# Kernel tuning notes

Hardware: AMD Instinct MI355X
Metric: run time of the kernel (lower is better)

## Reference

```python
import jax, jax.numpy as jnp
import numpy as np

B, S = 2, 2048
HID, NH, NKV, HD = 4096, 32, 8, 128
THETA = 10000.0
WINDOW = 1024  # sliding window size


def setup_inputs() -> dict:
    key = jax.random.key(0)
    k1, k2, k3 = jax.random.split(key, 3)
    hidden_states = jax.random.normal(k1, (B, S, HID), jnp.float32)
    wqkv = jax.random.normal(k2, (HID, (NH + 2 * NKV) * HD), jnp.float32) * 0.02
    wo = jax.random.normal(k3, (NH * HD, HID), jnp.float32) * 0.02
    positions = jnp.arange(S, dtype=jnp.int32)
    return {"hidden_states": hidden_states, "wqkv": wqkv, "wo": wo, "positions": positions}


def _rope_neox(x, positions):
    # x: [B, S, h, HD]; GPT-NeoX style: rotate concatenated halves.
    half = HD // 2
    inv_freq = 1.0 / (THETA ** (jnp.arange(half, dtype=jnp.float32) / half))
    ang = positions.astype(jnp.float32)[:, None] * inv_freq  # [S, half]
    cos = jnp.cos(ang)[None, :, None, :]
    sin = jnp.sin(ang)[None, :, None, :]
    x1, x2 = jnp.split(x, 2, axis=-1)
    return jnp.concatenate([x1 * cos - x2 * sin, x2 * cos + x1 * sin], axis=-1)


def reference(hidden_states, wqkv, wo, positions):
    qkv = hidden_states @ wqkv  # [B, S, (NH+2*NKV)*HD]
    q, k, v = jnp.split(qkv, [NH * HD, NH * HD + NKV * HD], axis=-1)
    q = q.reshape(B, S, NH, HD)
    k = k.reshape(B, S, NKV, HD)
    v = v.reshape(B, S, NKV, HD)
    q = _rope_neox(q, positions)
    k = _rope_neox(k, positions)
    # GQA: each KV head serves NH // NKV query heads
    rep = NH // NKV
    k = jnp.repeat(k, rep, axis=2)  # [B, S, NH, HD]
    v = jnp.repeat(v, rep, axis=2)
    scale = HD ** -0.5
    scores = jnp.einsum('bqhd,bkhd->bhqk', q, k) * scale  # [B, NH, S, S]
    i = jnp.arange(S)[:, None]
    j = jnp.arange(S)[None, :]
    mask = (j <= i) & (i - j < WINDOW)  # causal + sliding window
    scores = jnp.where(mask[None, None], scores, jnp.float32(-1e30))
    probs = jax.nn.softmax(scores, axis=-1)
    attn = jnp.einsum('bhqk,bkhd->bqhd', probs, v).reshape(B, S, NH * HD)
    return attn @ wo  # [B, S, HID]
```

## Files before the change

kernel.cpp:

```cpp
#include <hip/hip_runtime.h>


typedef __attribute__((ext_vector_type(8))) short short8;
typedef __attribute__((ext_vector_type(4))) float f32x4;
typedef __attribute__((ext_vector_type(16))) float f32x16;
typedef __attribute__((ext_vector_type(4))) unsigned int u32x4;
typedef __attribute__((ext_vector_type(4))) unsigned short u16x4;

__device__ __forceinline__ unsigned short f2bf(float f) {
  unsigned int u = __builtin_bit_cast(unsigned int, f);
  u = u + 0x7fffu + ((u >> 16) & 1u);
  return (unsigned short)(u >> 16);
}
__device__ __forceinline__ float bf2f(unsigned short h) {
  unsigned int u = ((unsigned int)h) << 16;
  return __builtin_bit_cast(float, u);
}
__device__ __forceinline__ unsigned int cvtpk_bf16(float lo, float hi) {
  unsigned int r;
  asm("v_cvt_pk_bf16_f32 %0, %1, %2" : "=v"(r) : "v"(lo), "v"(hi));
  return r;
}

__device__ __forceinline__ void gload_lds16(const unsigned short* g, unsigned short* l) {
  __builtin_amdgcn_global_load_lds(
      (const __attribute__((address_space(1))) unsigned int*)g,
      (__attribute__((address_space(3))) unsigned int*)l, 16, 0, 0);
}

#define MFMA16(A, B, C) __builtin_amdgcn_mfma_f32_16x16x32_bf16((A), (B), (C), 0, 0, 0)
#define MFMA32(A, B, C) __builtin_amdgcn_mfma_f32_32x32x16_bf16((A), (B), (C), 0, 0, 0)
#define BC8(x) __builtin_bit_cast(short8, (x))

__global__ __launch_bounds__(256) void cvt_plain(const float* __restrict__ in,
                                                 unsigned short* __restrict__ out, int n) {
  const int i = (blockIdx.x * 256 + threadIdx.x) * 4;
  (void)n;
  f32x4 v = *(const f32x4*)(in + i);
  u16x4 o;
#pragma unroll
  for (int j = 0; j < 4; ++j) o[j] = f2bf(v[j]);
  *(u16x4*)(out + i) = o;
}

__global__ __launch_bounds__(256) void cvt_t(const float* __restrict__ in,
                                             unsigned short* __restrict__ out,
                                             int R, int C) {
  __shared__ float t[32][33];
  const int c0 = blockIdx.x * 32, r0 = blockIdx.y * 32;
  const int tx = threadIdx.x & 31, ty = threadIdx.x >> 5;
#pragma unroll
  for (int i = 0; i < 4; ++i)
    t[ty + i * 8][tx] = in[(size_t)(r0 + ty + i * 8) * C + c0 + tx];
  __syncthreads();
#pragma unroll
  for (int i = 0; i < 4; ++i)
    out[(size_t)(c0 + ty + i * 8) * R + r0 + tx] = f2bf(t[tx][ty + i * 8]);
}

template <int NIF, int OUTF32>
__global__ __launch_bounds__(512, 2) void gemm256(const unsigned short* __restrict__ A,
                                                  const unsigned short* __restrict__ BT,
                                                  void* __restrict__ Cout,
                                                  int M, int N, int K) {
  constexpr int BUFE = 16384 + NIF * 4096;
  constexpr int NR = NIF + 4;
  __shared__ __align__(16) unsigned short lds[2][BUFE];
  const int tid = threadIdx.x;
  const int lane = tid & 63;
  const int w = tid >> 6;
  const int wr = w >> 2;
  const int wc = w & 3;
  const int g = lane >> 4;
  const int l15 = lane & 15;

  const int nwg = gridDim.x;
  const int cpx = nwg >> 3;
  const int bid = blockIdx.x;
  const int swz = (bid & 7) * cpx + (bid >> 3);
  const int MT = M >> 8;
  const int m0 = (swz % MT) * 256;
  const int n0 = (swz / MT) * (NIF * 64);

  const int lrow = lane >> 3;
  const int lcol = ((lane & 7) ^ lrow) * 8;
  const unsigned short* Asrc = A + (size_t)(m0 + w * 8 + lrow) * K + lcol;
  const unsigned short* Bsrc = BT + (size_t)(n0 + w * 8 + lrow) * K + lcol;

  f32x4 acc[8][NIF] = {};

  auto stage = [&](int buf, int t, int r) {
    if (r < NIF) {
      const int rb = r * 64;
      gload_lds16(Bsrc + (size_t)rb * K + t * 64,
                  &lds[buf][16384 + (rb + w * 8) * 64]);
    } else {
      const int j = r - NIF;
      const int rb = (j & 1) * 128 + ((j >> 1) & 1) * 64;
      gload_lds16(Asrc + (size_t)rb * K + t * 64,
                  &lds[buf][(rb + w * 8) * 64]);
    }
  };
  auto rdA = [&](int buf, int mi, int ks) {
    const int row = wr * 128 + mi * 16 + l15;
    const int cb = (ks * 64 + g * 16) ^ ((l15 & 7) << 4);
    return *(const u32x4*)((const char*)&lds[buf][0] + row * 128 + cb);
  };
  auto rdB = [&](int buf, int ni, int ks) {
    const int row = wc * (NIF * 16) + ni * 16 + l15;
    const int cb = (ks * 64 + g * 16) ^ ((l15 & 7) << 4);
    return *(const u32x4*)((const char*)&lds[buf][0] + 32768 + row * 128 + cb);
  };

#pragma unroll
  for (int r = 0; r < NR; ++r) stage(0, 0, r);
  asm volatile("s_waitcnt vmcnt(2)" ::: "memory");
  __builtin_amdgcn_sched_barrier(0);
  __builtin_amdgcn_s_barrier();

  const int NT = K >> 6;
  for (int t = 0; t < NT; ++t) {
    const int cb_ = t & 1, nb_ = cb_ ^ 1;
    const bool pre = (t + 1 < NT);
    u32x4 bfr[NIF][2];

    {
#pragma unroll
      for (int ni = 0; ni < NIF; ++ni) {
        bfr[ni][0] = rdB(cb_, ni, 0);
        bfr[ni][1] = rdB(cb_, ni, 1);
      }
      u32x4 a00 = rdA(cb_, 0, 0), a01 = rdA(cb_, 0, 1);
      u32x4 a10 = rdA(cb_, 1, 0), a11 = rdA(cb_, 1, 1);
      if (pre) { stage(nb_, t + 1, 0); stage(nb_, t + 1, 1); }
      __builtin_amdgcn_sched_barrier(0);
      __builtin_amdgcn_s_barrier();
      asm volatile("s_waitcnt lgkmcnt(0)" ::: "memory");
      __builtin_amdgcn_sched_barrier(0);
      __builtin_amdgcn_s_setprio(1);
#pragma unroll
      for (int ni = 0; ni < NIF; ++ni) {
        acc[0][ni] = MFMA16(BC8(a00), BC8(bfr[ni][0]), acc[0][ni]);
        acc[0][ni] = MFMA16(BC8(a01), BC8(bfr[ni][1]), acc[0][ni]);
        acc[1][ni] = MFMA16(BC8(a10), BC8(bfr[ni][0]), acc[1][ni]);
        acc[1][ni] = MFMA16(BC8(a11), BC8(bfr[ni][1]), acc[1][ni]);
      }
      __builtin_amdgcn_s_setprio(0);
      __builtin_amdgcn_sched_barrier(0);
      __builtin_amdgcn_s_barrier();
    }
    {
      u32x4 a00 = rdA(cb_, 2, 0), a01 = rdA(cb_, 2, 1);
      u32x4 a10 = rdA(cb_, 3, 0), a11 = rdA(cb_, 3, 1);
      if (pre) {
        stage(nb_, t + 1, 2); stage(nb_, t + 1, 3);
        asm volatile("s_waitcnt vmcnt(4)" ::: "memory");
      } else {
        asm volatile("s_waitcnt vmcnt(0)" ::: "memory");
      }
      __builtin_amdgcn_sched_barrier(0);
      __builtin_amdgcn_s_barrier();
      asm volatile("s_waitcnt lgkmcnt(0)" ::: "memory");
      __builtin_amdgcn_sched_barrier(0);
      __builtin_amdgcn_s_setprio(1);
#pragma unroll
      for (int ni = 0; ni < NIF; ++ni) {
        acc[2][ni] = MFMA16(BC8(a00), BC8(bfr[ni][0]), acc[2][ni]);
        acc[2][ni] = MFMA16(BC8(a01), BC8(bfr[ni][1]), acc[2][ni]);
        acc[3][ni] = MFMA16(BC8(a10), BC8(bfr[ni][0]), acc[3][ni]);
        acc[3][ni] = MFMA16(BC8(a11), BC8(bfr[ni][1]), acc[3][ni]);
      }
      __builtin_amdgcn_s_setprio(0);
      __builtin_amdgcn_sched_barrier(0);
      __builtin_amdgcn_s_barrier();
    }
    {
      u32x4 a00 = rdA(cb_, 4, 0), a01 = rdA(cb_, 4, 1);
      u32x4 a10 = rdA(cb_, 5, 0), a11 = rdA(cb_, 5, 1);
      if (pre) { stage(nb_, t + 1, 4); stage(nb_, t + 1, 5); }
      __builtin_amdgcn_sched_barrier(0);
      __builtin_amdgcn_s_barrier();
      asm volatile("s_waitcnt lgkmcnt(0)" ::: "memory");
      __builtin_amdgcn_sched_barrier(0);
      __builtin_amdgcn_s_setprio(1);
#pragma unroll
      for (int ni = 0; ni < NIF; ++ni) {
        acc[4][ni] = MFMA16(BC8(a00), BC8(bfr[ni][0]), acc[4][ni]);
        acc[4][ni] = MFMA16(BC8(a01), BC8(bfr[ni][1]), acc[4][ni]);
        acc[5][ni] = MFMA16(BC8(a10), BC8(bfr[ni][0]), acc[5][ni]);
        acc[5][ni] = MFMA16(BC8(a11), BC8(bfr[ni][1]), acc[5][ni]);
      }
      __builtin_amdgcn_s_setprio(0);
      __builtin_amdgcn_sched_barrier(0);
      __builtin_amdgcn_s_barrier();
    }
    {
      u32x4 a00 = rdA(cb_, 6, 0), a01 = rdA(cb_, 6, 1);
      u32x4 a10 = rdA(cb_, 7, 0), a11 = rdA(cb_, 7, 1);
      if (pre) {
        stage(nb_, t + 1, 6);
        if (NR == 8) stage(nb_, t + 1, 7);
        asm volatile("s_waitcnt vmcnt(2)" ::: "memory");
      }
      __builtin_amdgcn_sched_barrier(0);
      __builtin_amdgcn_s_barrier();
      asm volatile("s_waitcnt lgkmcnt(0)" ::: "memory");
      __builtin_amdgcn_sched_barrier(0);
      __builtin_amdgcn_s_setprio(1);
#pragma unroll
      for (int ni = 0; ni < NIF; ++ni) {
        acc[6][ni] = MFMA16(BC8(a00), BC8(bfr[ni][0]), acc[6][ni]);
        acc[6][ni] = MFMA16(BC8(a01), BC8(bfr[ni][1]), acc[6][ni]);
        acc[7][ni] = MFMA16(BC8(a10), BC8(bfr[ni][0]), acc[7][ni]);
        acc[7][ni] = MFMA16(BC8(a11), BC8(bfr[ni][1]), acc[7][ni]);
      }
      __builtin_amdgcn_s_setprio(0);
      __builtin_amdgcn_sched_barrier(0);
      __builtin_amdgcn_s_barrier();
    }
  }

  const int crow0 = m0 + wr * 128;
  const int ccol0 = n0 + wc * (NIF * 16);
#pragma unroll
  for (int mi = 0; mi < 8; ++mi)
#pragma unroll
    for (int ni = 0; ni < NIF; ++ni)
#pragma unroll
      for (int r = 0; r < 4; ++r) {
        const size_t idx =
            (size_t)(crow0 + mi * 16 + g * 4 + r) * N + (ccol0 + ni * 16 + l15);
        if constexpr (OUTF32) ((float*)Cout)[idx] = acc[mi][ni][r];
        else ((unsigned short*)Cout)[idx] = f2bf(acc[mi][ni][r]);
      }
}

__global__ __launch_bounds__(256) void rope_k(unsigned short* __restrict__ qkv,
                                              const int* __restrict__ pos) {
  const int idx = blockIdx.x * 256 + threadIdx.x;
  const int d = idx & 63;
  const int hh = (idx >> 6) & 7;
  const int tok = idx >> 9;
  const int s = tok & 2047;
  unsigned short* p = qkv + (size_t)tok * 6144 + 4096 + hh * 128 + d;
  const float x1 = bf2f(p[0]);
  const float x2 = bf2f(p[64]);
  const float inv = exp2f(-(float)d * 0.2076205059304601f);
  const float ang = (float)pos[s] * inv;
  const float c = cosf(ang), sn = sinf(ang);
  p[0]  = f2bf(x1 * c - x2 * sn);
  p[64] = f2bf(x2 * c + x1 * sn);
}

__global__ __launch_bounds__(512, 2) void attn_kernel(const unsigned short* __restrict__ qkv,
                                                      unsigned short* __restrict__ aout,
                                                      const int* __restrict__ pos) {
  __shared__ __align__(16) unsigned short smem[35840];

  const int tid = threadIdx.x;
  const int lane = tid & 63;
  const int w = tid >> 6;
  const int hi = lane >> 5;
  const int l31 = lane & 31;
  const int q0 = blockIdx.x * 256;
  const int h = blockIdx.y;
  const int b = blockIdx.z;
  const int kh = h >> 2;
  const size_t tokbase = (size_t)b * 2048;
  const int qw0 = q0 + w * 32;
  const int qg = qw0 + l31;

  short8 qf[8];
  {
    const unsigned short* qp = qkv + (tokbase + qg) * 6144 + h * 128;
#pragma unroll
    for (int ks8 = 0; ks8 < 8; ++ks8)
      qf[ks8] = BC8(*(const u32x4*)(qp + ks8 * 16 + hi * 8));
    const float fp = (float)pos[qg];
#pragma unroll
    for (int ks8 = 0; ks8 < 4; ++ks8)
#pragma unroll
      for (int j = 0; j < 8; ++j) {
        const int d = ks8 * 16 + hi * 8 + j;
        const float x1 = bf2f((unsigned short)qf[ks8][j]);
        const float x2 = bf2f((unsigned short)qf[ks8 + 4][j]);
        const float ang = fp * exp2f(-(float)d * 0.2076205059304601f);
        float c, sn;
        __sincosf(ang, &sn, &c);
        qf[ks8][j]     = (short)f2bf(x1 * c - x2 * sn);
        qf[ks8 + 4][j] = (short)f2bf(x2 * c + x1 * sn);
      }
  }

  const int c0key = tid >> 4, c0col = tid & 15;
  const int c1key = (tid + 512) >> 4, c1col = tid & 15;

  u32x4 kreg[2], vreg[2];
  const unsigned short* kvK = qkv + tokbase * 6144 + 4096 + kh * 128;

  const int t0 = (q0 >= 1024 ? (q0 - 1023) >> 6 : 0);
  const int t1 = (q0 + 255) >> 6;

  {
    const unsigned short* kb = kvK + (size_t)(t0 * 64) * 6144;
    kreg[0] = *(const u32x4*)(kb + (size_t)c0key * 6144 + c0col * 8);
    kreg[1] = *(const u32x4*)(kb + (size_t)c1key * 6144 + c1col * 8);
    vreg[0] = *(const u32x4*)(kb + (size_t)c0key * 6144 + 1024 + c0col * 8);
    vreg[1] = *(const u32x4*)(kb + (size_t)c1key * 6144 + 1024 + c1col * 8);
  }

  float m_run = -1e30f, l_run = 0.0f;
  f32x16 o_acc[4] = {};

  for (int kt = t0; kt <= t1; ++kt) {
    const int cur = (kt - t0) & 1;
    unsigned short* kdst = &smem[(cur)*17920];
    unsigned short* vdst = kdst + 8704;

    if (kt == t0) {
      *(u32x4*)&kdst[c0key * 136 + c0col * 8] = kreg[0];
      *(u32x4*)&kdst[c1key * 136 + c1col * 8] = kreg[1];
#pragma unroll
      for (int e = 0; e < 8; ++e) {
        const int e0 = (e + c0col) & 7;
        const int e1 = (e + c1col) & 7;
        vdst[(c0col * 8 + e0) * 72 + c0key] =
            (unsigned short)(vreg[0][e0 >> 1] >> ((e0 & 1) * 16));
        vdst[(c1col * 8 + e1) * 72 + c1key] =
            (unsigned short)(vreg[1][e1 >> 1] >> ((e1 & 1) * 16));
      }
      if (kt < t1) {
        const unsigned short* kb = kvK + (size_t)((kt + 1) * 64) * 6144;
        kreg[0] = *(const u32x4*)(kb + (size_t)c0key * 6144 + c0col * 8);
        kreg[1] = *(const u32x4*)(kb + (size_t)c1key * 6144 + c1col * 8);
        vreg[0] = *(const u32x4*)(kb + (size_t)c0key * 6144 + 1024 + c0col * 8);
        vreg[1] = *(const u32x4*)(kb + (size_t)c1key * 6144 + 1024 + c1col * 8);
      }
      __syncthreads();
    }

    if (kt < t1) {
      unsigned short* kdn = &smem[(cur ^ 1) * 17920];
      unsigned short* vdn = kdn + 8704;
      *(u32x4*)&kdn[c0key * 136 + c0col * 8] = kreg[0];
      *(u32x4*)&kdn[c1key * 136 + c1col * 8] = kreg[1];
#pragma unroll
      for (int e = 0; e < 8; ++e) {
        const int e0 = (e + c0col) & 7;
        const int e1 = (e + c1col) & 7;
        vdn[(c0col * 8 + e0) * 72 + c0key] =
            (unsigned short)(vreg[0][e0 >> 1] >> ((e0 & 1) * 16));
        vdn[(c1col * 8 + e1) * 72 + c1key] =
            (unsigned short)(vreg[1][e1 >> 1] >> ((e1 & 1) * 16));
      }
      if (kt + 2 <= t1) {
        const unsigned short* kb = kvK + (size_t)((kt + 2) * 64) * 6144;
        kreg[0] = *(const u32x4*)(kb + (size_t)c0key * 6144 + c0col * 8);
        kreg[1] = *(const u32x4*)(kb + (size_t)c1key * 6144 + c1col * 8);
        vreg[0] = *(const u32x4*)(kb + (size_t)c0key * 6144 + 1024 + c0col * 8);
        vreg[1] = *(const u32x4*)(kb + (size_t)c1key * 6144 + 1024 + c1col * 8);
      }
    }

    const int ktb = kt * 64;
    if (ktb <= qw0 + 31 && ktb + 63 >= qw0 - 1023) {
      const unsigned short* kb = &smem[cur * 17920];
      const unsigned short* vb = kb + 8704;

      f32x16 s0 = {}, s1 = {};
      const int arow = l31 * 136 + hi * 8;
#pragma unroll
      for (int ks8 = 0; ks8 < 8; ++ks8) {
        u32x4 a0 = *(const u32x4*)&kb[arow + ks8 * 16];
        u32x4 a1 = *(const u32x4*)&kb[arow + 32 * 136 + ks8 * 16];
        s0 = MFMA32(BC8(a0), qf[ks8], s0);
        s1 = MFMA32(BC8(a1), qf[ks8], s1);
      }

      const float scale = 0.08838834764831845f;
      float pv[32];
      const bool need_mask = !(ktb + 63 <= qw0 && ktb >= qw0 - 992);
      if (need_mask) {
#pragma unroll
        for (int r = 0; r < 16; ++r) {
          const int key0 = ktb + ((r & 3) + 8 * (r >> 2) + 4 * hi);
          const int key1 = key0 + 32;
          pv[r]      = (key0 <= qg && qg - key0 < 1024) ? s0[r] * scale : -1e30f;
          pv[16 + r] = (key1 <= qg && qg - key1 < 1024) ? s1[r] * scale : -1e30f;
        }
      } else {
#pragma unroll
        for (int r = 0; r < 16; ++r) {
          pv[r] = s0[r] * scale;
          pv[16 + r] = s1[r] * scale;
        }
      }

      float tm = -1e30f;
#pragma unroll
      for (int i = 0; i < 32; ++i) tm = fmaxf(tm, pv[i]);
      tm = fmaxf(tm, __shfl_xor(tm, 32, 64));
      if (__any(tm > m_run + 8.0f)) {
        const float mn = fmaxf(fmaxf(m_run, tm), -1e20f);
        const float scl = __expf(m_run - mn);
#pragma unroll
        for (int d = 0; d < 4; ++d) o_acc[d] *= scl;
        l_run *= scl;
        m_run = mn;
      }
      float lsum = 0.0f;
#pragma unroll
      for (int i = 0; i < 32; ++i) {
        pv[i] = __expf(pv[i] - m_run);
        lsum += pv[i];
      }
      l_run += lsum + __shfl_xor(lsum, 32, 64);

      u32x4 paf[4];
#pragma unroll
      for (int ks = 0; ks < 4; ++ks) {
        const int base = (ks >> 1) * 16 + (ks & 1) * 8;
        auto rA = __builtin_amdgcn_permlane32_swap(
            (int)cvtpk_bf16(pv[base + 0], pv[base + 1]),
            (int)cvtpk_bf16(pv[base + 4], pv[base + 5]), false, false);
        auto rB = __builtin_amdgcn_permlane32_swap(
            (int)cvtpk_bf16(pv[base + 2], pv[base + 3]),
            (int)cvtpk_bf16(pv[base + 6], pv[base + 7]), false, false);
        paf[ks][0] = (unsigned int)rA[0];
        paf[ks][1] = (unsigned int)rB[0];
        paf[ks][2] = (unsigned int)rA[1];
        paf[ks][3] = (unsigned int)rB[1];
      }

#pragma unroll
      for (int dblk = 0; dblk < 4; ++dblk) {
        const int vrow = (dblk * 32 + l31) * 72 + hi * 8;
#pragma unroll
        for (int ks = 0; ks < 4; ++ks) {
          u32x4 vf = *(const u32x4*)&vb[vrow + ks * 16];
          o_acc[dblk] = MFMA32(BC8(vf), BC8(paf[ks]), o_acc[dblk]);
        }
      }
    }

    __syncthreads();
  }

  const float rl = 1.0f / l_run;
  unsigned short* ob = &smem[w * 4352];
#pragma unroll
  for (int dblk = 0; dblk < 4; ++dblk)
#pragma unroll
    for (int rq = 0; rq < 4; ++rq) {
      u16x4 pk;
#pragma unroll
      for (int i = 0; i < 4; ++i) pk[i] = f2bf(o_acc[dblk][rq * 4 + i] * rl);
      *(u16x4*)&ob[l31 * 136 + dblk * 32 + rq * 8 + hi * 4] = pk;
    }
  __syncthreads();

  unsigned short* gout = aout + (tokbase + q0 + w * 32) * 4096 + h * 128;
#pragma unroll
  for (int r4 = 0; r4 < 8; ++r4) {
    const int row = r4 * 4 + (lane >> 4);
    u32x4 val = *(const u32x4*)&ob[row * 136 + (lane & 15) * 8];
    *(u32x4*)(gout + (size_t)row * 4096 + (lane & 15) * 8) = val;
  }
}

extern "C" void kernel_launch(void* const* d_in, const int* in_sizes, int n_in,
                              void* d_out, int out_size, void* d_ws, size_t ws_size,
                              hipStream_t stream) {
  (void)in_sizes; (void)n_in; (void)out_size; (void)ws_size;
  const float* hs   = (const float*)d_in[0];
  const float* wqkv = (const float*)d_in[1];
  const float* wo   = (const float*)d_in[2];
  const int*   pos  = (const int*)d_in[3];
  float* out = (float*)d_out;

  char* ws = (char*)d_ws;
  unsigned short* qkvb = (unsigned short*)ws;
  unsigned short* wT   = (unsigned short*)(ws + 50331648);
  unsigned short* hsb  = (unsigned short*)(ws + 100663296);

  cvt_t<<<dim3(6144 / 32, 4096 / 32), 256, 0, stream>>>(wqkv, wT, 4096, 6144);
  cvt_plain<<<16384, 256, 0, stream>>>(hs, hsb, 16777216);
  gemm256<3, 0><<<512, 512, 0, stream>>>(hsb, wT, qkvb, 4096, 6144, 4096);
  rope_k<<<8192, 256, 0, stream>>>(qkvb, pos);
  cvt_t<<<dim3(4096 / 32, 4096 / 32), 256, 0, stream>>>(wo, wT, 4096, 4096);
  attn_kernel<<<dim3(8, 32, 2), 512, 0, stream>>>(qkvb, hsb, pos);
  gemm256<4, 1><<<256, 512, 0, stream>>>(hsb, wT, out, 4096, 4096, 4096);
}
```

Baseline: 484.3 us.

## Merge conversion kernels, regroup GEMM phases, fold softmax scale into exp2

The two input conversion kernels are merged into one launch, and the K-RoPE kernel is merged with the wo transpose-convert. The GEMM main loop goes from four sub-phases of two M-fragments to three phases of 3/3/2, which cuts barriers and sched_barriers and lets more LDS reads be batched before the MFMAs. Attention folds scale*log2(e) into Q during RoPE and uses exp2f instead of __expf, removing a multiply per score. Removing the sched_barriers and explicit lgkmcnt waits leaves ordering to the compiler, which may change or break the intended overlap and register pressure.

```diff
diff --git a/kernel.cpp b/kernel.cpp
--- a/kernel.cpp
+++ b/kernel.cpp
@@ -32,30 +32,64 @@
 #define MFMA32(A, B, C) __builtin_amdgcn_mfma_f32_32x32x16_bf16((A), (B), (C), 0, 0, 0)
 #define BC8(x) __builtin_bit_cast(short8, (x))
 
-__global__ __launch_bounds__(256) void cvt_plain(const float* __restrict__ in,
-                                                 unsigned short* __restrict__ out, int n) {
-  const int i = (blockIdx.x * 256 + threadIdx.x) * 4;
-  (void)n;
-  f32x4 v = *(const f32x4*)(in + i);
-  u16x4 o;
-#pragma unroll
-  for (int j = 0; j < 4; ++j) o[j] = f2bf(v[j]);
-  *(u16x4*)(out + i) = o;
-}
-
-__global__ __launch_bounds__(256) void cvt_t(const float* __restrict__ in,
-                                             unsigned short* __restrict__ out,
-                                             int R, int C) {
-  __shared__ float t[32][33];
-  const int c0 = blockIdx.x * 32, r0 = blockIdx.y * 32;
-  const int tx = threadIdx.x & 31, ty = threadIdx.x >> 5;
-#pragma unroll
-  for (int i = 0; i < 4; ++i)
-    t[ty + i * 8][tx] = in[(size_t)(r0 + ty + i * 8) * C + c0 + tx];
-  __syncthreads();
-#pragma unroll
-  for (int i = 0; i < 4; ++i)
-    out[(size_t)(c0 + ty + i * 8) * R + r0 + tx] = f2bf(t[tx][ty + i * 8]);
+__global__ __launch_bounds__(256) void cvt1(const float* __restrict__ hs,
+                                            const float* __restrict__ wqkv,
+                                            unsigned short* __restrict__ hsb,
+                                            unsigned short* __restrict__ wT) {
+  const int bid = blockIdx.x;
+  if (bid < 24576) {
+    __shared__ float t[32][33];
+    const int c0 = (bid % 192) * 32, r0 = (bid / 192) * 32;
+    const int tx = threadIdx.x & 31, ty = threadIdx.x >> 5;
+#pragma unroll
+    for (int i = 0; i < 4; ++i)
+      t[ty + i * 8][tx] = wqkv[(size_t)(r0 + ty + i * 8) * 6144 + c0 + tx];
+    __syncthreads();
+#pragma unroll
+    for (int i = 0; i < 4; ++i)
+      wT[(size_t)(c0 + ty + i * 8) * 4096 + r0 + tx] = f2bf(t[tx][ty + i * 8]);
+  } else {
+    const int i = ((bid - 24576) * 256 + threadIdx.x) * 4;
+    f32x4 v = *(const f32x4*)(hs + i);
+    u16x4 o;
+#pragma unroll
+    for (int j = 0; j < 4; ++j) o[j] = f2bf(v[j]);
+    *(u16x4*)(hsb + i) = o;
+  }
+}
+
+__global__ __launch_bounds__(256) void rope_cvtwo(unsigned short* __restrict__ qkv,
+                                                  const int* __restrict__ pos,
+                                                  const float* __restrict__ wo,
+                                                  unsigned short* __restrict__ wT) {
+  const int bid = blockIdx.x;
+  if (bid < 8192) {
+    const int idx = bid * 256 + threadIdx.x;
+    const int d = idx & 63;
+    const int hh = (idx >> 6) & 7;
+    const int tok = idx >> 9;
+    const int s = tok & 2047;
+    unsigned short* p = qkv + (size_t)tok * 6144 + 4096 + hh * 128 + d;
+    const float x1 = bf2f(p[0]);
+    const float x2 = bf2f(p[64]);
+    const float inv = exp2f(-(float)d * 0.2076205059304601f);
+    const float ang = (float)pos[s] * inv;
+    const float c = cosf(ang), sn = sinf(ang);
+    p[0]  = f2bf(x1 * c - x2 * sn);
+    p[64] = f2bf(x2 * c + x1 * sn);
+  } else {
+    __shared__ float t[32][33];
+    const int b2 = bid - 8192;
+    const int c0 = (b2 % 128) * 32, r0 = (b2 / 128) * 32;
+    const int tx = threadIdx.x & 31, ty = threadIdx.x >> 5;
+#pragma unroll
+    for (int i = 0; i < 4; ++i)
+      t[ty + i * 8][tx] = wo[(size_t)(r0 + ty + i * 8) * 4096 + c0 + tx];
+    __syncthreads();
+#pragma unroll
+    for (int i = 0; i < 4; ++i)
+      wT[(size_t)(c0 + ty + i * 8) * 4096 + r0 + tx] = f2bf(t[tx][ty + i * 8]);
+  }
 }
 
 template <int NIF, int OUTF32>
@@ -115,7 +149,6 @@
 #pragma unroll
   for (int r = 0; r < NR; ++r) stage(0, 0, r);
   asm volatile("s_waitcnt vmcnt(2)" ::: "memory");
-  __builtin_amdgcn_sched_barrier(0);
   __builtin_amdgcn_s_barrier();
 
   const int NT = K >> 6;
@@ -130,92 +163,74 @@
         bfr[ni][0] = rdB(cb_, ni, 0);
         bfr[ni][1] = rdB(cb_, ni, 1);
       }
-      u32x4 a00 = rdA(cb_, 0, 0), a01 = rdA(cb_, 0, 1);
-      u32x4 a10 = rdA(cb_, 1, 0), a11 = rdA(cb_, 1, 1);
-      if (pre) { stage(nb_, t + 1, 0); stage(nb_, t + 1, 1); }
-      __builtin_amdgcn_sched_barrier(0);
-      __builtin_amdgcn_s_barrier();
-      asm volatile("s_waitcnt lgkmcnt(0)" ::: "memory");
-      __builtin_amdgcn_sched_barrier(0);
-      __builtin_amdgcn_s_setprio(1);
-#pragma unroll
-      for (int ni = 0; ni < NIF; ++ni) {
-        acc[0][ni] = MFMA16(BC8(a00), BC8(bfr[ni][0]), acc[0][ni]);
-        acc[0][ni] = MFMA16(BC8(a01), BC8(bfr[ni][1]), acc[0][ni]);
-        acc[1][ni] = MFMA16(BC8(a10), BC8(bfr[ni][0]), acc[1][ni]);
-        acc[1][ni] = MFMA16(BC8(a11), BC8(bfr[ni][1]), acc[1][ni]);
-      }
-      __builtin_amdgcn_s_setprio(0);
-      __builtin_amdgcn_sched_barrier(0);
-      __builtin_amdgcn_s_barrier();
-    }
-    {
-      u32x4 a00 = rdA(cb_, 2, 0), a01 = rdA(cb_, 2, 1);
-      u32x4 a10 = rdA(cb_, 3, 0), a11 = rdA(cb_, 3, 1);
+      u32x4 af[3][2];
+#pragma unroll
+      for (int mi = 0; mi < 3; ++mi) {
+        af[mi][0] = rdA(cb_, mi, 0);
+        af[mi][1] = rdA(cb_, mi, 1);
+      }
       if (pre) {
-        stage(nb_, t + 1, 2); stage(nb_, t + 1, 3);
-        asm volatile("s_waitcnt vmcnt(4)" ::: "memory");
+        stage(nb_, t + 1, 0); stage(nb_, t + 1, 1);
+        if (NIF == 4) stage(nb_, t + 1, 2);
+        asm volatile("s_waitcnt vmcnt(%0)" :: "i"(NIF == 4 ? 3 : 2) : "memory");
       } else {
         asm volatile("s_waitcnt vmcnt(0)" ::: "memory");
       }
-      __builtin_amdgcn_sched_barrier(0);
-      __builtin_amdgcn_s_barrier();
-      asm volatile("s_waitcnt lgkmcnt(0)" ::: "memory");
-      __builtin_amdgcn_sched_barrier(0);
+      __builtin_amdgcn_s_barrier();
       __builtin_amdgcn_s_setprio(1);
 #pragma unroll
-      for (int ni = 0; ni < NIF; ++ni) {
-        acc[2][ni] = MFMA16(BC8(a00), BC8(bfr[ni][0]), acc[2][ni]);
-        acc[2][ni] = MFMA16(BC8(a01), BC8(bfr[ni][1]), acc[2][ni]);
-        acc[3][ni] = MFMA16(BC8(a10), BC8(bfr[ni][0]), acc[3][ni]);
-        acc[3][ni] = MFMA16(BC8(a11), BC8(bfr[ni][1]), acc[3][ni]);
-      }
+      for (int mi = 0; mi < 3; ++mi)
+#pragma unroll
+        for (int ni = 0; ni < NIF; ++ni) {
+          acc[mi][ni] = MFMA16(BC8(af[mi][0]), BC8(bfr[ni][0]), acc[mi][ni]);
+          acc[mi][ni] = MFMA16(BC8(af[mi][1]), BC8(bfr[ni][1]), acc[mi][ni]);
+        }
       __builtin_amdgcn_s_setprio(0);
-      __builtin_amdgcn_sched_barrier(0);
       __builtin_amdgcn_s_barrier();
     }
     {
-      u32x4 a00 = rdA(cb_, 4, 0), a01 = rdA(cb_, 4, 1);
-      u32x4 a10 = rdA(cb_, 5, 0), a11 = rdA(cb_, 5, 1);
-      if (pre) { stage(nb_, t + 1, 4); stage(nb_, t + 1, 5); }
-      __builtin_amdgcn_sched_barrier(0);
-      __builtin_amdgcn_s_barrier();
-      asm volatile("s_waitcnt lgkmcnt(0)" ::: "memory");
-      __builtin_amdgcn_sched_barrier(0);
+      u32x4 af[3][2];
+#pragma unroll
+      for (int mi = 0; mi < 3; ++mi) {
+        af[mi][0] = rdA(cb_, 3 + mi, 0);
+        af[mi][1] = rdA(cb_, 3 + mi, 1);
+      }
+      if (pre) {
+        stage(nb_, t + 1, NR - 5); stage(nb_, t + 1, NR - 4); stage(nb_, t + 1, NR - 3);
+      }
+      __builtin_amdgcn_s_barrier();
       __builtin_amdgcn_s_setprio(1);
 #pragma unroll
-      for (int ni = 0; ni < NIF; ++ni) {
-        acc[4][ni] = MFMA16(BC8(a00), BC8(bfr[ni][0]), acc[4][ni]);
-        acc[4][ni] = MFMA16(BC8(a01), BC8(bfr[ni][1]), acc[4][ni]);
-        acc[5][ni] = MFMA16(BC8(a10), BC8(bfr[ni][0]), acc[5][ni]);
-        acc[5][ni] = MFMA16(BC8(a11), BC8(bfr[ni][1]), acc[5][ni]);
-      }
+      for (int mi = 0; mi < 3; ++mi)
+#pragma unroll
+        for (int ni = 0; ni < NIF; ++ni) {
+          acc[3 + mi][ni] = MFMA16(BC8(af[mi][0]), BC8(bfr[ni][0]), acc[3 + mi][ni]);
+          acc[3 + mi][ni] = MFMA16(BC8(af[mi][1]), BC8(bfr[ni][1]), acc[3 + mi][ni]);
+        }
       __builtin_amdgcn_s_setprio(0);
-      __builtin_amdgcn_sched_barrier(0);
       __builtin_amdgcn_s_barrier();
     }
     {
-      u32x4 a00 = rdA(cb_, 6, 0), a01 = rdA(cb_, 6, 1);
-      u32x4 a10 = rdA(cb_, 7, 0), a11 = rdA(cb_, 7, 1);
+      u32x4 af[2][2];
+#pragma unroll
+      for (int mi = 0; mi < 2; ++mi) {
+        af[mi][0] = rdA(cb_, 6 + mi, 0);
+        af[mi][1] = rdA(cb_, 6 + mi, 1);
+      }
       if (pre) {
-        stage(nb_, t + 1, 6);
-        if (NR == 8) stage(nb_, t + 1, 7);
+        stage(nb_, t + 1, NR - 2); stage(nb_, t + 1, NR - 1);
         asm volatile("s_waitcnt vmcnt(2)" ::: "memory");
       }
-      __builtin_amdgcn_sched_barrier(0);
-      __builtin_amdgcn_s_barrier();
-      asm volatile("s_waitcnt lgkmcnt(0)" ::: "memory");
-      __builtin_amdgcn_sched_barrier(0);
+      __builtin_amdgcn_s_barrier();
       __builtin_amdgcn_s_setprio(1);
 #pragma unroll
-      for (int ni = 0; ni < NIF; ++ni) {
-        acc[6][ni] = MFMA16(BC8(a00), BC8(bfr[ni][0]), acc[6][ni]);
-        acc[6][ni] = MFMA16(BC8(a01), BC8(bfr[ni][1]), acc[6][ni]);
-        acc[7][ni] = MFMA16(BC8(a10), BC8(bfr[ni][0]), acc[7][ni]);
-        acc[7][ni] = MFMA16(BC8(a11), BC8(bfr[ni][1]), acc[7][ni]);
-      }
+      for (int mi = 0; mi < 2; ++mi)
+#pragma unroll
+        for (int ni = 0; ni < NIF; ++ni) {
+          acc[6 + mi][ni] = MFMA16(BC8(af[mi][0]), BC8(bfr[ni][0]), acc[6 + mi][ni]);
+          acc[6 + mi][ni] = MFMA16(BC8(af[mi][1]), BC8(bfr[ni][1]), acc[6 + mi][ni]);
+        }
       __builtin_amdgcn_s_setprio(0);
-      __builtin_amdgcn_sched_barrier(0);
       __builtin_amdgcn_s_barrier();
     }
   }
@@ -233,23 +248,6 @@
         if constexpr (OUTF32) ((float*)Cout)[idx] = acc[mi][ni][r];
         else ((unsigned short*)Cout)[idx] = f2bf(acc[mi][ni][r]);
       }
-}
-
-__global__ __launch_bounds__(256) void rope_k(unsigned short* __restrict__ qkv,
-                                              const int* __restrict__ pos) {
-  const int idx = blockIdx.x * 256 + threadIdx.x;
-  const int d = idx & 63;
-  const int hh = (idx >> 6) & 7;
-  const int tok = idx >> 9;
-  const int s = tok & 2047;
-  unsigned short* p = qkv + (size_t)tok * 6144 + 4096 + hh * 128 + d;
-  const float x1 = bf2f(p[0]);
-  const float x2 = bf2f(p[64]);
-  const float inv = exp2f(-(float)d * 0.2076205059304601f);
-  const float ang = (float)pos[s] * inv;
-  const float c = cosf(ang), sn = sinf(ang);
-  p[0]  = f2bf(x1 * c - x2 * sn);
-  p[64] = f2bf(x2 * c + x1 * sn);
 }
 
 __global__ __launch_bounds__(512, 2) void attn_kernel(const unsigned short* __restrict__ qkv,
@@ -287,6 +285,7 @@
         const float ang = fp * exp2f(-(float)d * 0.2076205059304601f);
         float c, sn;
         __sincosf(ang, &sn, &c);
+        c *= 0.12751743f; sn *= 0.12751743f;
         qf[ks8][j]     = (short)f2bf(x1 * c - x2 * sn);
         qf[ks8 + 4][j] = (short)f2bf(x2 * c + x1 * sn);
       }
@@ -377,7 +376,6 @@
         s1 = MFMA32(BC8(a1), qf[ks8], s1);
       }
 
-      const float scale = 0.08838834764831845f;
       float pv[32];
       const bool need_mask = !(ktb + 63 <= qw0 && ktb >= qw0 - 992);
       if (need_mask) {
@@ -385,14 +383,14 @@
         for (int r = 0; r < 16; ++r) {
           const int key0 = ktb + ((r & 3) + 8 * (r >> 2) + 4 * hi);
           const int key1 = key0 + 32;
-          pv[r]      = (key0 <= qg && qg - key0 < 1024) ? s0[r] * scale : -1e30f;
-          pv[16 + r] = (key1 <= qg && qg - key1 < 1024) ? s1[r] * scale : -1e30f;
+          pv[r]      = (key0 <= qg && qg - key0 < 1024) ? s0[r] : -1e30f;
+          pv[16 + r] = (key1 <= qg && qg - key1 < 1024) ? s1[r] : -1e30f;
         }
       } else {
 #pragma unroll
         for (int r = 0; r < 16; ++r) {
-          pv[r] = s0[r] * scale;
-          pv[16 + r] = s1[r] * scale;
+          pv[r] = s0[r];
+          pv[16 + r] = s1[r];
         }
       }
 
@@ -400,9 +398,9 @@
 #pragma unroll
       for (int i = 0; i < 32; ++i) tm = fmaxf(tm, pv[i]);
       tm = fmaxf(tm, __shfl_xor(tm, 32, 64));
-      if (__any(tm > m_run + 8.0f)) {
+      if (__any(tm > m_run + 11.5415603f)) {
         const float mn = fmaxf(fmaxf(m_run, tm), -1e20f);
-        const float scl = __expf(m_run - mn);
+        const float scl = exp2f(m_run - mn);
 #pragma unroll
         for (int d = 0; d < 4; ++d) o_acc[d] *= scl;
         l_run *= scl;
@@ -411,7 +409,7 @@
       float lsum = 0.0f;
 #pragma unroll
       for (int i = 0; i < 32; ++i) {
-        pv[i] = __expf(pv[i] - m_run);
+        pv[i] = exp2f(pv[i] - m_run);
         lsum += pv[i];
       }
       l_run += lsum + __shfl_xor(lsum, 32, 64);
@@ -483,11 +481,9 @@
   unsigned short* wT   = (unsigned short*)(ws + 50331648);
   unsigned short* hsb  = (unsigned short*)(ws + 100663296);
 
-  cvt_t<<<dim3(6144 / 32, 4096 / 32), 256, 0, stream>>>(wqkv, wT, 4096, 6144);
-  cvt_plain<<<16384, 256, 0, stream>>>(hs, hsb, 16777216);
+  cvt1<<<40960, 256, 0, stream>>>(hs, wqkv, hsb, wT);
   gemm256<3, 0><<<512, 512, 0, stream>>>(hsb, wT, qkvb, 4096, 6144, 4096);
-  rope_k<<<8192, 256, 0, stream>>>(qkvb, pos);
-  cvt_t<<<dim3(4096 / 32, 4096 / 32), 256, 0, stream>>>(wo, wT, 4096, 4096);
+  rope_cvtwo<<<24576, 256, 0, stream>>>(qkvb, pos, wo, wT);
   attn_kernel<<<dim3(8, 32, 2), 512, 0, stream>>>(qkvb, hsb, pos);
   gemm256<4, 1><<<256, 512, 0, stream>>>(hsb, wT, out, 4096, 4096, 4096);
 }
```

After: 489.0 us. About the same (+1.0%).
